# Optimization experiments

Measured on AMD Instinct MI355X. Metric: run time of the kernel, lower is better.

The kernel has to match this reference:

```python
import jax, jax.numpy as jnp
import numpy as np

N_NODES = 50000
N_EDGES = 800000
IN_DIM = 128
HID = 64
OUT_DIM = 128
N_GRAPHS = 128


def setup_inputs() -> dict:
    key = jax.random.key(0)
    ks = jax.random.split(key, 16)

    def lin(k, fan_in, fan_out):
        k1, k2 = jax.random.split(k)
        bound = 1.0 / np.sqrt(fan_in)
        W = jax.random.uniform(k1, (fan_in, fan_out), jnp.float32, -bound, bound)
        b = jax.random.uniform(k2, (fan_out,), jnp.float32, -bound, bound)
        return W, b

    x = jax.random.normal(ks[0], (N_NODES, IN_DIM), jnp.float32)
    edge_index = jax.random.randint(ks[1], (2, N_EDGES), 0, N_NODES, jnp.int64)
    batch = jnp.sort(jax.random.randint(ks[2], (N_NODES,), 0, N_GRAPHS, jnp.int64))

    W_in, b_in = lin(ks[3], IN_DIM, HID)
    W1_0, b1_0 = lin(ks[4], HID, HID)
    W2_0, b2_0 = lin(ks[5], HID, HID)
    W1_1, b1_1 = lin(ks[6], HID, HID)
    W2_1, b2_1 = lin(ks[7], HID, HID)
    W_out, b_out = lin(ks[8], HID, OUT_DIM)

    return dict(x=x, edge_index=edge_index, batch=batch,
                W_in=W_in, b_in=b_in,
                W1_0=W1_0, b1_0=b1_0, W2_0=W2_0, b2_0=b2_0,
                W1_1=W1_1, b1_1=b1_1, W2_1=W2_1, b2_1=b2_1,
                W_out=W_out, b_out=b_out)


def _gin_conv(x, src, dst, W1, b1, W2, b2):
    # aggr[i] = sum_{(s,i) in E} x[s]; GIN (eps=0): h = MLP(x + aggr)
    msgs = x[src]  # [E, HID] gather
    aggr = jax.ops.segment_sum(msgs, dst, num_segments=N_NODES)
    h = x + aggr
    h = jax.nn.relu(h @ W1 + b1)
    return h @ W2 + b2


def reference(x, edge_index, batch,
              W_in, b_in,
              W1_0, b1_0, W2_0, b2_0,
              W1_1, b1_1, W2_1, b2_1,
              W_out, b_out):
    src, dst = edge_index[0], edge_index[1]
    h = x @ W_in + b_in  # proj_in
    # conv 0 (+ReLU; dropout is identity in eval mode)
    h = jax.nn.relu(_gin_conv(h, src, dst, W1_0, b1_0, W2_0, b2_0))
    # conv 1
    h = jax.nn.relu(_gin_conv(h, src, dst, W1_1, b1_1, W2_1, b2_1))
    h = h @ W_out + b_out  # proj_out -> [N, OUT_DIM]
    # global mean pool over graphs
    sums = jax.ops.segment_sum(h, batch, num_segments=N_GRAPHS)
    counts = jax.ops.segment_sum(jnp.ones((h.shape[0],), h.dtype), batch, num_segments=N_GRAPHS)
    graph_emb = sums / jnp.maximum(counts, 1.0)[:, None]  # [N_GRAPHS, OUT_DIM]
    return graph_emb
```

## Files before the change

kernel.cpp:

```cpp
#include <hip/hip_runtime.h>
#include <hip/hip_fp16.h>

#define N_NODES   50000
#define N_EDGES   800000
#define IN_DIM    128
#define HID       64
#define OUT_DIM   128
#define N_GRAPHS  128

#define NBKT      196
#define BBLK      392
#define BSTRIDE   5120
#define CAP       40

#define OFF_GCUR   0
#define OFF_GSUM   196
#define OFF_GSTART 8388
#define OFF_ROWPTR 8518
#define OFF_SRCL   58520
#define OFF_EPAIRS 458520
#define OFF_HA     1462040
#define OFF_HB     2262040
#define OFF_WT     3062040

typedef float v2f __attribute__((ext_vector_type(2)));
typedef float f32x4 __attribute__((ext_vector_type(4)));
typedef short bf16x8 __attribute__((ext_vector_type(8)));

union FragU { uint4 u; bf16x8 v; };

__device__ __forceinline__ unsigned short f2bf(float f) {
    union { float f; unsigned int u; } v; v.f = f;
    const unsigned int r = v.u + 0x7FFFu + ((v.u >> 16) & 1u);
    return (unsigned short)(r >> 16);
}

__device__ __forceinline__ void acc_fp8x8(float acc[8], const uint2 w) {
    const v2f a = __builtin_amdgcn_cvt_pk_f32_fp8(w.x, false);
    const v2f b = __builtin_amdgcn_cvt_pk_f32_fp8(w.x, true);
    const v2f c = __builtin_amdgcn_cvt_pk_f32_fp8(w.y, false);
    const v2f d = __builtin_amdgcn_cvt_pk_f32_fp8(w.y, true);
    acc[0] += a.x; acc[1] += a.y; acc[2] += b.x; acc[3] += b.y;
    acc[4] += c.x; acc[5] += c.y; acc[6] += d.x; acc[7] += d.y;
}

__device__ __forceinline__ uint2 pack_fp8x8(const float f[8]) {
    int w0 = 0, w1 = 0;
    w0 = __builtin_amdgcn_cvt_pk_fp8_f32(f[0], f[1], w0, false);
    w0 = __builtin_amdgcn_cvt_pk_fp8_f32(f[2], f[3], w0, true);
    w1 = __builtin_amdgcn_cvt_pk_fp8_f32(f[4], f[5], w1, false);
    w1 = __builtin_amdgcn_cvt_pk_fp8_f32(f[6], f[7], w1, true);
    uint2 r; r.x = (unsigned)w0; r.y = (unsigned)w1;
    return r;
}

#define BG_SMEM_BYTES 32144

__device__ __forceinline__ void role_bucket(char* smem, const int* __restrict__ ei,
                                            int* __restrict__ gcur,
                                            unsigned int* __restrict__ epairs,
                                            int bid) {
    int* lcnt = (int*)smem;
    unsigned int* stage = (unsigned int*)(smem + NBKT * 4);
    const int t = threadIdx.x;
    for (int i = t; i < NBKT; i += 256) lcnt[i] = 0;
    __syncthreads();
    for (int e0 = bid * 512; e0 < N_EDGES; e0 += BBLK * 512) {
#pragma unroll
        for (int half = 0; half < 2; ++half) {
            const int e = e0 + half * 256 + t;
            if (e < N_EDGES) {
                const unsigned int src = (unsigned int)ei[e];
                const unsigned int dst = (unsigned int)ei[N_EDGES + e];
                const int b = dst >> 8;
                const unsigned int pk = src | (dst << 16);
                const int pos = atomicAdd(&lcnt[b], 1);
                if (pos < CAP) stage[b * CAP + pos] = pk;
                else {
                    const int gp = atomicAdd(&gcur[b], 1);
                    epairs[b * BSTRIDE + gp] = pk;
                }
            }
        }
        __syncthreads();
        if (t < NBKT) {
            int n = lcnt[t]; if (n > CAP) n = CAP;
            if (n >= 16) {
                const int f = n & ~15;
                const int base = atomicAdd(&gcur[t], f);
                if ((base & 3) == 0) {
                    for (int i = 0; i < f; i += 4)
                        *(uint4*)&epairs[t * BSTRIDE + base + i] =
                            *(const uint4*)&stage[t * CAP + i];
                } else {
                    for (int i = 0; i < f; ++i)
                        epairs[t * BSTRIDE + base + i] = stage[t * CAP + i];
                }
                for (int i = 0; i < n - f; ++i)
                    stage[t * CAP + i] = stage[t * CAP + f + i];
                lcnt[t] = n - f;
            } else {
                lcnt[t] = n;
            }
        }
        __syncthreads();
    }
    if (t < NBKT) {
        const int n = lcnt[t];
        if (n > 0) {
            const int base = atomicAdd(&gcur[t], n);
            for (int i = 0; i < n; ++i)
                epairs[t * BSTRIDE + base + i] = stage[t * CAP + i];
        }
    }
}

__device__ __forceinline__ void role_gbound(const int* __restrict__ batch,
                                            int* __restrict__ gstart, int bid) {
    const int n = bid * 256 + threadIdx.x;
    if (n >= N_NODES) return;
    const int b = batch[n];
    if (n == 0) {
        for (int g = 0; g <= b; ++g) gstart[g] = 0;
    } else {
        const int p = batch[n - 1];
        for (int g = p + 1; g <= b; ++g) gstart[g] = n;
    }
    if (n == N_NODES - 1) {
        for (int g = b + 1; g <= N_GRAPHS; ++g) gstart[g] = N_NODES;
    }
}

__device__ __forceinline__ void role_wprep(const float* __restrict__ Wi,
                                           const float* __restrict__ W10,
                                           const float* __restrict__ W20,
                                           const float* __restrict__ W11,
                                           const float* __restrict__ W21,
                                           unsigned short* __restrict__ wtg) {
    const int t = threadIdx.x;
    for (int i = t; i < 128 * 64; i += 256) {
        const int k = i >> 6, c = i & 63;
        wtg[c * 136 + k] = f2bf(Wi[i]);
    }
    const float* Ws[4] = {W10, W20, W11, W21};
#pragma unroll
    for (int m = 0; m < 4; ++m) {
        unsigned short* o = wtg + 8704 + m * 4608;
        const float* w = Ws[m];
        for (int i = t; i < 64 * 64; i += 256) {
            const int k = i >> 6, c = i & 63;
            o[c * 72 + k] = f2bf(w[i]);
        }
    }
}

__global__ __launch_bounds__(256) void k_bg(
        const int* __restrict__ ei, const int* __restrict__ batch,
        int* __restrict__ gcur, unsigned int* __restrict__ epairs,
        int* __restrict__ gstart,
        const float* __restrict__ Wi, const float* __restrict__ W10,
        const float* __restrict__ W20, const float* __restrict__ W11,
        const float* __restrict__ W21, unsigned short* __restrict__ wtg) {
    __shared__ __attribute__((aligned(16))) char smem[BG_SMEM_BYTES];
    const int bid = blockIdx.x;
    if (bid < BBLK)              role_bucket(smem, ei, gcur, epairs, bid);
    else if (bid < BBLK + NBKT)  role_gbound(batch, gstart, bid - BBLK);
    else                         role_wprep(Wi, W10, W20, W11, W21, wtg);
}

#define CP_SMEM_BYTES 34816

__device__ __forceinline__ void role_csr(char* smem, const int* __restrict__ gcur,
                                         const unsigned int* __restrict__ epairs,
                                         int* __restrict__ rowptr,
                                         unsigned short* __restrict__ srclist, int b) {
    int* lhist = (int*)smem;
    int* lcur  = lhist + 256;
    int* pws   = lcur + 256;
    int* wtot  = pws + 4;
    int* lsrc  = wtot + 4;
    const int t = threadIdx.x;
    const int lane = t & 63, wv = t >> 6;

    int po = 0;
    for (int j = t; j < b; j += 256) po += gcur[j];
#pragma unroll
    for (int m = 32; m; m >>= 1) po += __shfl_xor(po, m, 64);
    if (lane == 0) pws[wv] = po;
    lhist[t] = 0;
    __syncthreads();
    const int base = pws[0] + pws[1] + pws[2] + pws[3];
    const int cnt = gcur[b];

    for (int i = t; i < cnt; i += 256)
        atomicAdd(&lhist[(epairs[b * BSTRIDE + i] >> 16) & 255], 1);
    __syncthreads();

    const int d = lhist[t];
    int incl = d;
#pragma unroll
    for (int off = 1; off < 64; off <<= 1) {
        const int u = __shfl_up(incl, off, 64);
        if (lane >= off) incl += u;
    }
    if (lane == 63) wtot[wv] = incl;
    __syncthreads();
    int woff = 0;
#pragma unroll
    for (int i = 0; i < 4; ++i) woff += (i < wv) ? wtot[i] : 0;
    const int excl = woff + incl - d;
    lcur[t] = excl;
    const int node = b * 256 + t;
    if (node < N_NODES) rowptr[node] = base + excl;
    if (b == NBKT - 1 && t == 0) rowptr[N_NODES] = base + cnt;
    __syncthreads();

    for (int i = t; i < cnt; i += 256) {
        const unsigned int u = epairs[b * BSTRIDE + i];
        const int pos = atomicAdd(&lcur[(u >> 16) & 255], 1);
        lsrc[pos] = (int)(u & 0xFFFFu);
    }
    __syncthreads();
    for (int i = t; i < cnt; i += 256)
        srclist[base + i] = (unsigned short)lsrc[i];
}

__device__ __forceinline__ void role_proj(char* smem, const float* __restrict__ x,
                                          const unsigned short* __restrict__ Wt_g,
                                          const float* __restrict__ b,
                                          unsigned char* __restrict__ h8, int bid) {
    unsigned short* X16 = (unsigned short*)smem;
    unsigned short* Wt  = (unsigned short*)(smem + 17408);
    float* OUT32 = (float*)smem;
    const int t = threadIdx.x;
    const int nb = bid * 64;
    {
        const uint4* s = (const uint4*)Wt_g;
        uint4* d = (uint4*)Wt;
        for (int i = t; i < 1088; i += 256) d[i] = s[i];
    }
    for (int i = t; i < 64 * (IN_DIM / 4); i += 256) {
        const int n = i >> 5;
        const int k4 = (i & 31) * 4;
        float4 val = make_float4(0.f, 0.f, 0.f, 0.f);
        if (nb + n < N_NODES)
            val = *(const float4*)(x + (size_t)(nb + n) * IN_DIM + k4);
        union { uint2 u; unsigned short s[4]; } pk;
        pk.s[0] = f2bf(val.x); pk.s[1] = f2bf(val.y);
        pk.s[2] = f2bf(val.z); pk.s[3] = f2bf(val.w);
        *(uint2*)&X16[n * 136 + k4] = pk.u;
    }
    __syncthreads();

    const int l = t & 63;
    const int m0 = (t >> 6) * 16;
    const int lrow = l & 15;
    const int lk = (l >> 4) * 8;
    FragU a[4];
#pragma unroll
    for (int s = 0; s < 4; ++s)
        a[s].u = *(const uint4*)&X16[(m0 + lrow) * 136 + s * 32 + lk];
    f32x4 acc[4];
#pragma unroll
    for (int n = 0; n < 4; ++n) {
        const float bv = b[n * 16 + lrow];
        acc[n] = (f32x4){bv, bv, bv, bv};
#pragma unroll
        for (int s = 0; s < 4; ++s) {
            FragU w;
            w.u = *(const uint4*)&Wt[(n * 16 + lrow) * 136 + s * 32 + lk];
            acc[n] = __builtin_amdgcn_mfma_f32_16x16x32_bf16(a[s].v, w.v, acc[n], 0, 0, 0);
        }
    }
    __syncthreads();
#pragma unroll
    for (int n = 0; n < 4; ++n)
#pragma unroll
        for (int r = 0; r < 4; ++r)
            OUT32[(m0 + (l >> 4) * 4 + r) * 68 + n * 16 + lrow] = acc[n][r];
    __syncthreads();
    const int ln = t & 31;
    const int c0 = (t >> 5) * 8;
#pragma unroll
    for (int j = 0; j < 2; ++j) {
        const int n = nb + ln + 32 * j;
        if (n < N_NODES) {
            float f[8];
            const float* src = &OUT32[(ln + 32 * j) * 68 + c0];
            *(float4*)&f[0] = *(const float4*)&src[0];
            *(float4*)&f[4] = *(const float4*)&src[4];
            const uint2 p = pack_fp8x8(f);
            *(uint2*)(h8 + (size_t)n * HID + c0) = p;
        }
    }
}

__global__ __launch_bounds__(256) void k_cp(
        const int* __restrict__ gcur, const unsigned int* __restrict__ epairs,
        const float* __restrict__ x, const unsigned short* __restrict__ Wt_g,
        const float* __restrict__ b,
        int* __restrict__ rowptr, unsigned short* __restrict__ srcl,
        unsigned char* __restrict__ h8) {
    __shared__ __attribute__((aligned(16))) char smem[CP_SMEM_BYTES];
    const int bid = blockIdx.x;
    if (bid < NBKT) role_csr(smem, gcur, epairs, rowptr, srcl, bid);
    else            role_proj(smem, x, Wt_g, b, h8, bid - NBKT);
}

#define S_AB 72
template<int POOL>
__global__ __launch_bounds__(256, 4) void k_conv_t(
        const unsigned char* __restrict__ hin8,
        const int* __restrict__ rowptr, const unsigned short* __restrict__ srclist,
        const unsigned short* __restrict__ W1t_g, const float* __restrict__ b1,
        const unsigned short* __restrict__ W2t_g, const float* __restrict__ b2,
        unsigned char* __restrict__ hout8,
        const int* __restrict__ batch, float* __restrict__ gsum) {
    __shared__ __attribute__((aligned(16))) char csm[36864];
    unsigned short* A16 = (unsigned short*)csm;
    unsigned short* H16 = (unsigned short*)(csm + 9216);
    unsigned short* W1t = (unsigned short*)(csm + 18432);
    unsigned short* W2t = (unsigned short*)(csm + 27648);
    float* OUT32 = (float*)csm;
    const int t = threadIdx.x;
    {
        const uint4* s1 = (const uint4*)W1t_g;
        const uint4* s2 = (const uint4*)W2t_g;
        uint4* d1 = (uint4*)W1t;
        uint4* d2 = (uint4*)W2t;
        for (int i = t; i < 576; i += 256) { d1[i] = s1[i]; d2[i] = s2[i]; }
    }

    const int nb = blockIdx.x * 64;
    const int grp = t >> 3;
    const int q = t & 7;
#pragma unroll
    for (int pass = 0; pass < 2; ++pass) {
        const int nloc = pass * 32 + grp;
        const int node = nb + nloc;
        float acc[8] = {0.f, 0.f, 0.f, 0.f, 0.f, 0.f, 0.f, 0.f};
        if (node < N_NODES) {
            acc_fp8x8(acc, *(const uint2*)(hin8 + (size_t)node * HID + q * 8));
            const int beg = rowptr[node];
            const int end = rowptr[node + 1];
            int e = beg;
            for (; e + 8 <= end; e += 8) {
                int s[8];
#pragma unroll
                for (int i = 0; i < 8; ++i) s[i] = srclist[e + i];
                uint2 r[8];
#pragma unroll
                for (int i = 0; i < 8; ++i)
                    r[i] = *(const uint2*)(hin8 + (size_t)s[i] * HID + q * 8);
#pragma unroll
                for (int i = 0; i < 8; ++i) acc_fp8x8(acc, r[i]);
            }
            for (; e < end; ++e)
                acc_fp8x8(acc, *(const uint2*)(hin8 + (size_t)srclist[e] * HID + q * 8));
        }
        union { uint4 u; unsigned short s[8]; } ou;
#pragma unroll
        for (int c = 0; c < 8; ++c) ou.s[c] = f2bf(acc[c]);
        *(uint4*)&A16[nloc * S_AB + q * 8] = ou.u;
    }
    __syncthreads();

    const int l = t & 63;
    const int m0 = (t >> 6) * 16;
    const int lrow = l & 15;
    const int lk = (l >> 4) * 8;

    FragU a0, a1;
    a0.u = *(const uint4*)&A16[(m0 + lrow) * S_AB + lk];
    a1.u = *(const uint4*)&A16[(m0 + lrow) * S_AB + 32 + lk];
    f32x4 acc1[4];
#pragma unroll
    for (int n = 0; n < 4; ++n) {
        const float bv = b1[n * 16 + lrow];
        acc1[n] = (f32x4){bv, bv, bv, bv};
        FragU w0, w1;
        w0.u = *(const uint4*)&W1t[(n * 16 + lrow) * S_AB + lk];
        w1.u = *(const uint4*)&W1t[(n * 16 + lrow) * S_AB + 32 + lk];
        acc1[n] = __builtin_amdgcn_mfma_f32_16x16x32_bf16(a0.v, w0.v, acc1[n], 0, 0, 0);
        acc1[n] = __builtin_amdgcn_mfma_f32_16x16x32_bf16(a1.v, w1.v, acc1[n], 0, 0, 0);
    }
    __syncthreads();
#pragma unroll
    for (int n = 0; n < 4; ++n)
#pragma unroll
        for (int r = 0; r < 4; ++r) {
            const int row = m0 + (l >> 4) * 4 + r;
            H16[row * S_AB + n * 16 + lrow] = f2bf(fmaxf(acc1[n][r], 0.0f));
        }
    __syncthreads();

    FragU h0, h1;
    h0.u = *(const uint4*)&H16[(m0 + lrow) * S_AB + lk];
    h1.u = *(const uint4*)&H16[(m0 + lrow) * S_AB + 32 + lk];
    f32x4 acc2[4];
#pragma unroll
    for (int n = 0; n < 4; ++n) {
        const float bv = b2[n * 16 + lrow];
        acc2[n] = (f32x4){bv, bv, bv, bv};
        FragU w0, w1;
        w0.u = *(const uint4*)&W2t[(n * 16 + lrow) * S_AB + lk];
        w1.u = *(const uint4*)&W2t[(n * 16 + lrow) * S_AB + 32 + lk];
        acc2[n] = __builtin_amdgcn_mfma_f32_16x16x32_bf16(h0.v, w0.v, acc2[n], 0, 0, 0);
        acc2[n] = __builtin_amdgcn_mfma_f32_16x16x32_bf16(h1.v, w1.v, acc2[n], 0, 0, 0);
    }
    __syncthreads();
#pragma unroll
    for (int n = 0; n < 4; ++n)
#pragma unroll
        for (int r = 0; r < 4; ++r)
            OUT32[(m0 + (l >> 4) * 4 + r) * 68 + n * 16 + lrow] = fmaxf(acc2[n][r], 0.0f);
    __syncthreads();

    const int ln = t & 31;
    const int c0 = (t >> 5) * 8;
    if constexpr (POOL) {
        const int nlast = (nb + 64 <= N_NODES) ? nb + 63 : N_NODES - 1;
        const int g0 = batch[nb];
        const int g1 = batch[nlast];
        int myg[2];
        float f[2][8];
#pragma unroll
        for (int j = 0; j < 2; ++j) {
            const int n = nb + ln + 32 * j;
            myg[j] = (n < N_NODES) ? batch[n] : -1;
            const float* src = &OUT32[(ln + 32 * j) * 68 + c0];
            *(float4*)&f[j][0] = *(const float4*)&src[0];
            *(float4*)&f[j][4] = *(const float4*)&src[4];
        }
        for (int g = g0; g <= g1; ++g) {
#pragma unroll
            for (int j = 0; j < 2; ++j) {
#pragma unroll
                for (int c = 0; c < 8; ++c) {
                    float v = (myg[j] == g) ? f[j][c] : 0.0f;
#pragma unroll
                    for (int m = 16; m; m >>= 1) v += __shfl_xor(v, m, 64);
                    if (ln == 0) atomicAdd(&gsum[g * HID + c0 + c], v);
                }
            }
        }
    } else {
#pragma unroll
        for (int j = 0; j < 2; ++j) {
            const int n = nb + ln + 32 * j;
            if (n < N_NODES) {
                float f[8];
                const float* src = &OUT32[(ln + 32 * j) * 68 + c0];
                *(float4*)&f[0] = *(const float4*)&src[0];
                *(float4*)&f[4] = *(const float4*)&src[4];
                const uint2 p = pack_fp8x8(f);
                *(uint2*)(hout8 + (size_t)n * HID + c0) = p;
            }
        }
    }
}

__global__ __launch_bounds__(128) void k_out(
        const float* __restrict__ gsum, const int* __restrict__ gstart,
        const float* __restrict__ Wo, const float* __restrict__ bo,
        float* __restrict__ out) {
    __shared__ float mean[HID];
    const int g = blockIdx.x;
    const int t = threadIdx.x;
    const int cnt = gstart[g + 1] - gstart[g];
    if (t < HID)
        mean[t] = (cnt > 0) ? gsum[g * HID + t] / (float)cnt : 0.0f;
    __syncthreads();
    float o = 0.0f;
    for (int k = 0; k < HID; ++k)
        o = fmaf(mean[k], Wo[k * OUT_DIM + t], o);
    out[g * OUT_DIM + t] = (cnt > 0) ? o + bo[t] : 0.0f;
}

extern "C" void kernel_launch(void* const* d_in, const int* in_sizes, int n_in,
                              void* d_out, int out_size, void* d_ws, size_t ws_size,
                              hipStream_t stream) {
    const float* x     = (const float*)d_in[0];
    const int*   ei    = (const int*)d_in[1];
    const int*   batch = (const int*)d_in[2];
    const float* W_in  = (const float*)d_in[3];
    const float* b_in  = (const float*)d_in[4];
    const float* W1_0  = (const float*)d_in[5];
    const float* b1_0  = (const float*)d_in[6];
    const float* W2_0  = (const float*)d_in[7];
    const float* b2_0  = (const float*)d_in[8];
    const float* W1_1  = (const float*)d_in[9];
    const float* b1_1  = (const float*)d_in[10];
    const float* W2_1  = (const float*)d_in[11];
    const float* b2_1  = (const float*)d_in[12];
    const float* W_out = (const float*)d_in[13];
    const float* b_out = (const float*)d_in[14];
    float* out = (float*)d_out;

    unsigned int*   wsw    = (unsigned int*)d_ws;
    int*            gcur   = (int*)(wsw + OFF_GCUR);
    float*          gsum   = (float*)(wsw + OFF_GSUM);
    int*            gstart = (int*)(wsw + OFF_GSTART);
    int*            rowptr = (int*)(wsw + OFF_ROWPTR);
    unsigned short* srcl   = (unsigned short*)(wsw + OFF_SRCL);
    unsigned int*   epairs = (unsigned int*)(wsw + OFF_EPAIRS);
    unsigned char*  hA     = (unsigned char*)(wsw + OFF_HA);
    unsigned char*  hB     = (unsigned char*)(wsw + OFF_HB);
    unsigned short* wtg    = (unsigned short*)(wsw + OFF_WT);

    unsigned short* wt_in = wtg;
    unsigned short* wt10  = wtg + 8704;
    unsigned short* wt20  = wtg + 13312;
    unsigned short* wt11  = wtg + 17920;
    unsigned short* wt21  = wtg + 22528;

    const int pi_blocks = (N_NODES + 63) / 64;
    const int cv_blocks = (N_NODES + 63) / 64;
    const int bg_blocks = BBLK + NBKT + 1;
    const int cp_blocks = NBKT + pi_blocks;

    hipMemsetAsync(gcur, 0, (NBKT + N_GRAPHS * HID) * sizeof(int), stream);
    k_bg<<<bg_blocks, 256, 0, stream>>>(ei, batch, gcur, epairs, gstart,
                                        W_in, W1_0, W2_0, W1_1, W2_1, wtg);
    k_cp<<<cp_blocks, 256, 0, stream>>>(gcur, epairs, x, wt_in, b_in,
                                        rowptr, srcl, hA);
    k_conv_t<0><<<cv_blocks, 256, 0, stream>>>(hA, rowptr, srcl,
                                               wt10, b1_0, wt20, b2_0, hB,
                                               batch, gsum);
    k_conv_t<1><<<cv_blocks, 256, 0, stream>>>(hB, rowptr, srcl,
                                               wt11, b1_1, wt21, b2_1, hA,
                                               batch, gsum);
    k_out<<<N_GRAPHS, 128, 0, stream>>>(gsum, gstart, W_out, b_out, out);
}
```

Before: 187.2 us.

## Move input projection into bucketing kernel and split CSR build into own kernel

The input projection blocks move from the CSR kernel into the first kernel, so they run alongside edge bucketing. The CSR build becomes a standalone small kernel. Each projection block now converts W_in to bf16 in shared memory itself instead of copying a pre-converted global copy. The bucketing loop also drops its per-iteration flush and barriers, relying on a slightly larger stage capacity plus the global-atomic overflow path. The trade-off is redundant weight conversion in every projection block, larger shared memory for all first-kernel blocks, and more global atomics if buckets overflow.

```diff
diff --git a/kernel.cpp b/kernel.cpp
--- a/kernel.cpp
+++ b/kernel.cpp
@@ -11,7 +11,7 @@
 #define NBKT      196
 #define BBLK      392
 #define BSTRIDE   5120
-#define CAP       40
+#define CAP       42
 
 #define OFF_GCUR   0
 #define OFF_GSUM   196
@@ -54,7 +54,7 @@
     return r;
 }
 
-#define BG_SMEM_BYTES 32144
+#define K1_SMEM_BYTES 34816
 
 __device__ __forceinline__ void role_bucket(char* smem, const int* __restrict__ ei,
                                             int* __restrict__ gcur,
@@ -82,31 +82,10 @@
                 }
             }
         }
-        __syncthreads();
-        if (t < NBKT) {
-            int n = lcnt[t]; if (n > CAP) n = CAP;
-            if (n >= 16) {
-                const int f = n & ~15;
-                const int base = atomicAdd(&gcur[t], f);
-                if ((base & 3) == 0) {
-                    for (int i = 0; i < f; i += 4)
-                        *(uint4*)&epairs[t * BSTRIDE + base + i] =
-                            *(const uint4*)&stage[t * CAP + i];
-                } else {
-                    for (int i = 0; i < f; ++i)
-                        epairs[t * BSTRIDE + base + i] = stage[t * CAP + i];
-                }
-                for (int i = 0; i < n - f; ++i)
-                    stage[t * CAP + i] = stage[t * CAP + f + i];
-                lcnt[t] = n - f;
-            } else {
-                lcnt[t] = n;
-            }
-        }
-        __syncthreads();
-    }
+    }
+    __syncthreads();
     if (t < NBKT) {
-        const int n = lcnt[t];
+        int n = lcnt[t]; if (n > CAP) n = CAP;
         if (n > 0) {
             const int base = atomicAdd(&gcur[t], n);
             for (int i = 0; i < n; ++i)
@@ -131,17 +110,12 @@
     }
 }
 
-__device__ __forceinline__ void role_wprep(const float* __restrict__ Wi,
-                                           const float* __restrict__ W10,
+__device__ __forceinline__ void role_wprep(const float* __restrict__ W10,
                                            const float* __restrict__ W20,
                                            const float* __restrict__ W11,
                                            const float* __restrict__ W21,
                                            unsigned short* __restrict__ wtg) {
     const int t = threadIdx.x;
-    for (int i = t; i < 128 * 64; i += 256) {
-        const int k = i >> 6, c = i & 63;
-        wtg[c * 136 + k] = f2bf(Wi[i]);
-    }
     const float* Ws[4] = {W10, W20, W11, W21};
 #pragma unroll
     for (int m = 0; m < 4; ++m) {
@@ -154,79 +128,8 @@
     }
 }
 
-__global__ __launch_bounds__(256) void k_bg(
-        const int* __restrict__ ei, const int* __restrict__ batch,
-        int* __restrict__ gcur, unsigned int* __restrict__ epairs,
-        int* __restrict__ gstart,
-        const float* __restrict__ Wi, const float* __restrict__ W10,
-        const float* __restrict__ W20, const float* __restrict__ W11,
-        const float* __restrict__ W21, unsigned short* __restrict__ wtg) {
-    __shared__ __attribute__((aligned(16))) char smem[BG_SMEM_BYTES];
-    const int bid = blockIdx.x;
-    if (bid < BBLK)              role_bucket(smem, ei, gcur, epairs, bid);
-    else if (bid < BBLK + NBKT)  role_gbound(batch, gstart, bid - BBLK);
-    else                         role_wprep(Wi, W10, W20, W11, W21, wtg);
-}
-
-#define CP_SMEM_BYTES 34816
-
-__device__ __forceinline__ void role_csr(char* smem, const int* __restrict__ gcur,
-                                         const unsigned int* __restrict__ epairs,
-                                         int* __restrict__ rowptr,
-                                         unsigned short* __restrict__ srclist, int b) {
-    int* lhist = (int*)smem;
-    int* lcur  = lhist + 256;
-    int* pws   = lcur + 256;
-    int* wtot  = pws + 4;
-    int* lsrc  = wtot + 4;
-    const int t = threadIdx.x;
-    const int lane = t & 63, wv = t >> 6;
-
-    int po = 0;
-    for (int j = t; j < b; j += 256) po += gcur[j];
-#pragma unroll
-    for (int m = 32; m; m >>= 1) po += __shfl_xor(po, m, 64);
-    if (lane == 0) pws[wv] = po;
-    lhist[t] = 0;
-    __syncthreads();
-    const int base = pws[0] + pws[1] + pws[2] + pws[3];
-    const int cnt = gcur[b];
-
-    for (int i = t; i < cnt; i += 256)
-        atomicAdd(&lhist[(epairs[b * BSTRIDE + i] >> 16) & 255], 1);
-    __syncthreads();
-
-    const int d = lhist[t];
-    int incl = d;
-#pragma unroll
-    for (int off = 1; off < 64; off <<= 1) {
-        const int u = __shfl_up(incl, off, 64);
-        if (lane >= off) incl += u;
-    }
-    if (lane == 63) wtot[wv] = incl;
-    __syncthreads();
-    int woff = 0;
-#pragma unroll
-    for (int i = 0; i < 4; ++i) woff += (i < wv) ? wtot[i] : 0;
-    const int excl = woff + incl - d;
-    lcur[t] = excl;
-    const int node = b * 256 + t;
-    if (node < N_NODES) rowptr[node] = base + excl;
-    if (b == NBKT - 1 && t == 0) rowptr[N_NODES] = base + cnt;
-    __syncthreads();
-
-    for (int i = t; i < cnt; i += 256) {
-        const unsigned int u = epairs[b * BSTRIDE + i];
-        const int pos = atomicAdd(&lcur[(u >> 16) & 255], 1);
-        lsrc[pos] = (int)(u & 0xFFFFu);
-    }
-    __syncthreads();
-    for (int i = t; i < cnt; i += 256)
-        srclist[base + i] = (unsigned short)lsrc[i];
-}
-
 __device__ __forceinline__ void role_proj(char* smem, const float* __restrict__ x,
-                                          const unsigned short* __restrict__ Wt_g,
+                                          const float* __restrict__ Wi,
                                           const float* __restrict__ b,
                                           unsigned char* __restrict__ h8, int bid) {
     unsigned short* X16 = (unsigned short*)smem;
@@ -234,10 +137,9 @@
     float* OUT32 = (float*)smem;
     const int t = threadIdx.x;
     const int nb = bid * 64;
-    {
-        const uint4* s = (const uint4*)Wt_g;
-        uint4* d = (uint4*)Wt;
-        for (int i = t; i < 1088; i += 256) d[i] = s[i];
+    for (int i = t; i < 128 * 64; i += 256) {
+        const int k = i >> 6, c = i & 63;
+        Wt[c * 136 + k] = f2bf(Wi[i]);
     }
     for (int i = t; i < 64 * (IN_DIM / 4); i += 256) {
         const int n = i >> 5;
@@ -295,16 +197,79 @@
     }
 }
 
-__global__ __launch_bounds__(256) void k_cp(
+__global__ __launch_bounds__(256) void k_bg(
+        const int* __restrict__ ei, const int* __restrict__ batch,
+        int* __restrict__ gcur, unsigned int* __restrict__ epairs,
+        int* __restrict__ gstart,
+        const float* __restrict__ x, const float* __restrict__ Wi,
+        const float* __restrict__ bi, unsigned char* __restrict__ hA,
+        const float* __restrict__ W10, const float* __restrict__ W20,
+        const float* __restrict__ W11, const float* __restrict__ W21,
+        unsigned short* __restrict__ wtg) {
+    __shared__ __attribute__((aligned(16))) char smem[K1_SMEM_BYTES];
+    const int bid = blockIdx.x;
+    if (bid < BBLK)                   role_bucket(smem, ei, gcur, epairs, bid);
+    else if (bid < BBLK + NBKT)       role_gbound(batch, gstart, bid - BBLK);
+    else if (bid == BBLK + NBKT)      role_wprep(W10, W20, W11, W21, wtg);
+    else                              role_proj(smem, x, Wi, bi, hA, bid - (BBLK + NBKT + 1));
+}
+
+#define CSR_SMEM_BYTES 22560
+
+__global__ __launch_bounds__(256) void k_csr(
         const int* __restrict__ gcur, const unsigned int* __restrict__ epairs,
-        const float* __restrict__ x, const unsigned short* __restrict__ Wt_g,
-        const float* __restrict__ b,
-        int* __restrict__ rowptr, unsigned short* __restrict__ srcl,
-        unsigned char* __restrict__ h8) {
-    __shared__ __attribute__((aligned(16))) char smem[CP_SMEM_BYTES];
-    const int bid = blockIdx.x;
-    if (bid < NBKT) role_csr(smem, gcur, epairs, rowptr, srcl, bid);
-    else            role_proj(smem, x, Wt_g, b, h8, bid - NBKT);
+        int* __restrict__ rowptr, unsigned short* __restrict__ srclist) {
+    __shared__ __attribute__((aligned(16))) char smem[CSR_SMEM_BYTES];
+    int* lhist = (int*)smem;
+    int* lcur  = lhist + 256;
+    int* pws   = lcur + 256;
+    int* wtot  = pws + 4;
+    int* lsrc  = wtot + 4;
+    const int b = blockIdx.x;
+    const int t = threadIdx.x;
+    const int lane = t & 63, wv = t >> 6;
+
+    int po = 0;
+    for (int j = t; j < b; j += 256) po += gcur[j];
+#pragma unroll
+    for (int m = 32; m; m >>= 1) po += __shfl_xor(po, m, 64);
+    if (lane == 0) pws[wv] = po;
+    lhist[t] = 0;
+    __syncthreads();
+    const int base = pws[0] + pws[1] + pws[2] + pws[3];
+    const int cnt = gcur[b];
+
+    for (int i = t; i < cnt; i += 256)
+        atomicAdd(&lhist[(epairs[b * BSTRIDE + i] >> 16) & 255], 1);
+    __syncthreads();
+
+    const int d = lhist[t];
+    int incl = d;
+#pragma unroll
+    for (int off = 1; off < 64; off <<= 1) {
+        const int u = __shfl_up(incl, off, 64);
+        if (lane >= off) incl += u;
+    }
+    if (lane == 63) wtot[wv] = incl;
+    __syncthreads();
+    int woff = 0;
+#pragma unroll
+    for (int i = 0; i < 4; ++i) woff += (i < wv) ? wtot[i] : 0;
+    const int excl = woff + incl - d;
+    lcur[t] = excl;
+    const int node = b * 256 + t;
+    if (node < N_NODES) rowptr[node] = base + excl;
+    if (b == NBKT - 1 && t == 0) rowptr[N_NODES] = base + cnt;
+    __syncthreads();
+
+    for (int i = t; i < cnt; i += 256) {
+        const unsigned int u = epairs[b * BSTRIDE + i];
+        const int pos = atomicAdd(&lcur[(u >> 16) & 255], 1);
+        lsrc[pos] = (int)(u & 0xFFFFu);
+    }
+    __syncthreads();
+    for (int i = t; i < cnt; i += 256)
+        srclist[base + i] = (unsigned short)lsrc[i];
 }
 
 #define S_AB 72
@@ -508,7 +473,6 @@
     unsigned char*  hB     = (unsigned char*)(wsw + OFF_HB);
     unsigned short* wtg    = (unsigned short*)(wsw + OFF_WT);
 
-    unsigned short* wt_in = wtg;
     unsigned short* wt10  = wtg + 8704;
     unsigned short* wt20  = wtg + 13312;
     unsigned short* wt11  = wtg + 17920;
@@ -516,14 +480,13 @@
 
     const int pi_blocks = (N_NODES + 63) / 64;
     const int cv_blocks = (N_NODES + 63) / 64;
-    const int bg_blocks = BBLK + NBKT + 1;
-    const int cp_blocks = NBKT + pi_blocks;
+    const int bg_blocks = BBLK + NBKT + 1 + pi_blocks;
 
     hipMemsetAsync(gcur, 0, (NBKT + N_GRAPHS * HID) * sizeof(int), stream);
     k_bg<<<bg_blocks, 256, 0, stream>>>(ei, batch, gcur, epairs, gstart,
-                                        W_in, W1_0, W2_0, W1_1, W2_1, wtg);
-    k_cp<<<cp_blocks, 256, 0, stream>>>(gcur, epairs, x, wt_in, b_in,
-                                        rowptr, srcl, hA);
+                                        x, W_in, b_in, hA,
+                                        W1_0, W2_0, W1_1, W2_1, wtg);
+    k_csr<<<NBKT, 256, 0, stream>>>(gcur, epairs, rowptr, srcl);
     k_conv_t<0><<<cv_blocks, 256, 0, stream>>>(hA, rowptr, srcl,
                                                wt10, b1_0, wt20, b2_0, hB,
                                                batch, gsum);
```

Measured after the change: 175.3 us. -6.3%, faster.
